# Kernel tuning notes

Measured on AMD Instinct MI355X. Metric: run time of the kernel, lower is better.

## Reference

```python
import jax, jax.numpy as jnp
import numpy as np

DIM = 512; NB = 4; BS = DIM // NB            # EinFFT blocks
DS = 64; DC = 4; EXP = 2; DI = EXP * DIM      # Mamba dims
DTR = DIM // 16                               # dt_rank
BLOCKS = 2; LAM = 0.01; B_SZ = 2; L_SZ = 1024

def layer_norm(x, w, b):
    m = x.mean(-1, keepdims=True)
    v = x.var(-1, keepdims=True)
    return (x - m) / jnp.sqrt(v + 1e-5) * w + b

def softshrink(x, lam):
    return jnp.where(x > lam, x - lam, jnp.where(x < -lam, x + lam, jnp.zeros((), x.dtype)))

def mamba(x, in_proj_w, conv_w, conv_b, x_proj_w, dt_proj_w, dt_proj_b, A_log, D, out_proj_w):
    B, L, _ = x.shape
    xz = x @ in_proj_w.T                      # (B,L,2*DI)
    xm, z = jnp.split(xz, 2, axis=-1)
    # causal depthwise conv1d, keep first L outputs
    xt = xm.transpose(0, 2, 1)                # (B,DI,L)
    conv = jax.lax.conv_general_dilated(xt, conv_w, (1,), [(DC - 1, 0)],
                                        feature_group_count=DI,
                                        dimension_numbers=('NCH', 'OIH', 'NCH'))
    xm = jax.nn.silu((conv + conv_b[None, :, None]).transpose(0, 2, 1))  # (B,L,DI)
    proj = xm @ x_proj_w.T                    # (B,L,DTR+2*DS)
    dt = proj[..., :DTR]
    Bm = proj[..., DTR:DTR + DS]
    Cm = proj[..., DTR + DS:]
    dt = jax.nn.softplus(dt @ dt_proj_w.T + dt_proj_b)   # (B,L,DI)
    A = -jnp.exp(A_log)                       # (DI,DS)

    def step(h, inp):
        dt_t, B_t, C_t, u_t = inp             # (B,DI),(B,DS),(B,DS),(B,DI)
        dA = jnp.exp(dt_t[:, :, None] * A)
        h = dA * h + dt_t[:, :, None] * B_t[:, None, :] * u_t[:, :, None]
        y = jnp.einsum('bds,bs->bd', h, C_t)
        return h, y

    h0 = jnp.zeros((B, DI, DS), x.dtype)
    _, ys = jax.lax.scan(step, h0, (dt.transpose(1, 0, 2), Bm.transpose(1, 0, 2),
                                    Cm.transpose(1, 0, 2), xm.transpose(1, 0, 2)))
    y = ys.transpose(1, 0, 2) + xm * D        # (B,L,DI)
    y = y * jax.nn.silu(z)
    return y @ out_proj_w.T

def einfft(x, cw1, cw2, cb1, cb2):
    B, N, C = x.shape
    xf = jnp.fft.fft2(x.reshape(B, N, NB, BS), axes=(1, 2), norm='ortho')
    mul = lambda t, w: jnp.einsum('BNbd,bdk->BNbk', t, w)
    r1 = jax.nn.relu(mul(xf.real, cw1[0]) - mul(xf.imag, cw1[1]) + cb1[0])
    i1 = jax.nn.relu(mul(xf.real, cw1[1]) + mul(xf.imag, cw1[0]) + cb1[1])
    r2 = softshrink(mul(r1, cw2[0]) - mul(i1, cw2[1]) + cb2[0], LAM)
    i2 = softshrink(mul(r1, cw2[1]) + mul(i1, cw2[0]) + cb2[1], LAM)
    out = jnp.fft.ifft2(r2 + 1j * i2, axes=(1, 2), norm='ortho')
    return out.real.astype(x.dtype).reshape(B, N, C)

def setup_inputs() -> dict:
    key = jax.random.key(0)
    ks = jax.random.split(key, 16)
    r = lambda i, shape, s: jax.random.normal(ks[i], shape, jnp.float32) * s
    A_log = jnp.log(jnp.tile(jnp.arange(1, DS + 1, dtype=jnp.float32), (DI, 1)))
    return {
        'x': jax.random.normal(ks[0], (B_SZ, L_SZ, DIM), jnp.float32),
        'ln_w': jnp.ones((DIM,), jnp.float32), 'ln_b': jnp.zeros((DIM,), jnp.float32),
        'in_proj_w': r(1, (2 * DI, DIM), 0.02),
        'conv_w': r(2, (DI, 1, DC), 0.1), 'conv_b': jnp.zeros((DI,), jnp.float32),
        'x_proj_w': r(3, (DTR + 2 * DS, DI), 0.02),
        'dt_proj_w': r(4, (DI, DTR), 0.02),
        'dt_proj_b': jnp.full((DI,), float(np.log(np.expm1(0.01))), jnp.float32),
        'A_log': A_log, 'D': jnp.ones((DI,), jnp.float32),
        'out_proj_w': r(5, (DIM, DI), 0.02),
        'norm2_w': jnp.ones((DIM,), jnp.float32), 'norm2_b': jnp.zeros((DIM,), jnp.float32),
        'cw1': r(6, (2, NB, BS, BS), 0.02), 'cw2': r(7, (2, NB, BS, BS), 0.02),
        'cb1': r(8, (2, NB, BS), 0.02), 'cb2': r(9, (2, NB, BS), 0.02),
    }

def reference(x, ln_w, ln_b, in_proj_w, conv_w, conv_b, x_proj_w, dt_proj_w, dt_proj_b,
              A_log, D, out_proj_w, norm2_w, norm2_b, cw1, cw2, cb1, cb2):
    for _ in range(BLOCKS):
        x = x + mamba(layer_norm(x, ln_w, ln_b), in_proj_w, conv_w, conv_b,
                      x_proj_w, dt_proj_w, dt_proj_b, A_log, D, out_proj_w)
        x = x + einfft(layer_norm(x, norm2_w, norm2_b), cw1, cw2, cb1, cb2)
    return x
```

## Files before the change

### kernel.cpp

```cpp
#include <hip/hip_runtime.h>

typedef unsigned short u16;
typedef __attribute__((ext_vector_type(8))) short bf8;
typedef __attribute__((ext_vector_type(4))) float f4;

__device__ __forceinline__ float bf2f(u16 b) {
    return __uint_as_float(((unsigned)b) << 16);
}
__device__ __forceinline__ u16 f2bf(float f) {
    unsigned u = __float_as_uint(f);
    u += 0x7fffu + ((u >> 16) & 1u);
    return (u16)(u >> 16);
}
__device__ __forceinline__ void pack8f(const float* v, u16* dst) {
    uint r0 = (uint)f2bf(v[0]) | ((uint)f2bf(v[1]) << 16);
    uint r1 = (uint)f2bf(v[2]) | ((uint)f2bf(v[3]) << 16);
    uint r2 = (uint)f2bf(v[4]) | ((uint)f2bf(v[5]) << 16);
    uint r3 = (uint)f2bf(v[6]) | ((uint)f2bf(v[7]) << 16);
    *(uint4*)dst = make_uint4(r0, r1, r2, r3);
}
__device__ __forceinline__ void pack8u(const u16* v, u16* dst) {
    uint r0 = (uint)v[0] | ((uint)v[1] << 16);
    uint r1 = (uint)v[2] | ((uint)v[3] << 16);
    uint r2 = (uint)v[4] | ((uint)v[5] << 16);
    uint r3 = (uint)v[6] | ((uint)v[7] << 16);
    *(uint4*)dst = make_uint4(r0, r1, r2, r3);
}
__device__ __forceinline__ bf8 neg8(bf8 v) {
    union { bf8 b; uint u[4]; } t; t.b = v;
    t.u[0] ^= 0x80008000u; t.u[1] ^= 0x80008000u;
    t.u[2] ^= 0x80008000u; t.u[3] ^= 0x80008000u;
    return t.b;
}

__global__ void detect_k(const u16* __restrict__ dtb, int* __restrict__ flag) {
    flag[0] = (dtb[0] == dtb[1] && dtb[1] == dtb[2] && dtb[2] == dtb[3] &&
               dtb[3] == dtb[4] && dtb[4] == dtb[5]) ? 1 : 0;
    flag[1] = 1;
}

__global__ __launch_bounds__(256)
void achk_k(const float* __restrict__ alog, int* __restrict__ flag) {
    int i = blockIdx.x * 256 + threadIdx.x;
    int s = i & 63;
    float n = __expf(alog[i]);
    float e = (float)(s + 1);
    if (fabsf(n - e) > 0.02f * e) atomicAnd(&flag[1], 0);
}

struct CvtArgs {
    const void* src[18];
    void* dst[18];
    int n[18];
    int obf[18];
};
__global__ __launch_bounds__(256)
void cvt_all_k(CvtArgs a, const int* __restrict__ flag) {
    const int t = blockIdx.y;
    const int n = a.n[t];
    const int f = flag[0];
    if (a.obf[t]) {
        u16* __restrict__ d = (u16*)a.dst[t];
        if (f) {
            const u16* __restrict__ s = (const u16*)a.src[t];
            for (int i = blockIdx.x * 256 + threadIdx.x; i < n; i += gridDim.x * 256)
                d[i] = s[i];
        } else {
            const float* __restrict__ s = (const float*)a.src[t];
            for (int i = blockIdx.x * 256 + threadIdx.x; i < n; i += gridDim.x * 256)
                d[i] = f2bf(s[i]);
        }
    } else {
        float* __restrict__ d = (float*)a.dst[t];
        if (f) {
            const u16* __restrict__ s = (const u16*)a.src[t];
            for (int i = blockIdx.x * 256 + threadIdx.x; i < n; i += gridDim.x * 256)
                d[i] = bf2f(s[i]);
        } else {
            const float* __restrict__ s = (const float*)a.src[t];
            for (int i = blockIdx.x * 256 + threadIdx.x; i < n; i += gridDim.x * 256)
                d[i] = s[i];
        }
    }
}

__global__ void out_k(const float* __restrict__ in, void* __restrict__ out,
                      int n, const int* __restrict__ flag) {
    int i = blockIdx.x * 256 + threadIdx.x;
    if (i >= n) return;
    if (flag[0]) ((u16*)out)[i] = f2bf(in[i]);
    else         ((float*)out)[i] = in[i];
}

__global__ void fgen_k(u16* __restrict__ Fr, u16* __restrict__ Fi) {
    int idx = blockIdx.x * 256 + threadIdx.x;
    int k = idx >> 10, n = idx & 1023;
    int m = (k * n) & 1023;
    float th = (float)m * (-6.283185307179586f / 1024.f);
    float s, c;
    __sincosf(th, &s, &c);
    Fr[idx] = f2bf(c * 0.03125f);
    Fi[idx] = f2bf(s * 0.03125f);
}

__global__ void wtr_k(const float* __restrict__ src, u16* __restrict__ dst) {
    int idx = blockIdx.x * 256 + threadIdx.x;
    int cin = idx & 127, cout = (idx >> 7) & 127, snb = idx >> 14;
    dst[(snb << 14) + (cout << 7) + cin] = f2bf(src[(snb << 14) + (cin << 7) + cout]);
}

__global__ __launch_bounds__(256)
void ln_k(const float* __restrict__ x, const float* __restrict__ w,
          const float* __restrict__ b, u16* __restrict__ out) {
    const int row = blockIdx.x, tid = threadIdx.x;
    const float* xr = x + (long)row * 512;
    float v0 = xr[tid], v1 = xr[tid + 256];
    float s = v0 + v1, q = v0 * v0 + v1 * v1;
#pragma unroll
    for (int off = 32; off; off >>= 1) {
        s += __shfl_xor(s, off);
        q += __shfl_xor(q, off);
    }
    __shared__ float ss[4], qq[4];
    int wid = tid >> 6;
    if ((tid & 63) == 0) { ss[wid] = s; qq[wid] = q; }
    __syncthreads();
    s = ss[0] + ss[1] + ss[2] + ss[3];
    q = qq[0] + qq[1] + qq[2] + qq[3];
    float mean = s * (1.f / 512.f);
    float var = q * (1.f / 512.f) - mean * mean;
    float rstd = rsqrtf(var + 1e-5f);
    u16* o = out + (long)row * 512;
    o[tid]       = f2bf((v0 - mean) * rstd * w[tid]       + b[tid]);
    o[tid + 256] = f2bf((v1 - mean) * rstd * w[tid + 256] + b[tid + 256]);
}

#define LSTR 40
template <int TAF, int EPI>
__global__ __launch_bounds__(256)
void mgemm_k(const void* __restrict__ Ap, const u16* __restrict__ Bp,
             float* __restrict__ D, int N, int K, int lda, int ldb, int ldc,
             const float* __restrict__ bias, const float* __restrict__ res) {
    const float* Af = (const float*)Ap;
    const u16*  Ab  = (const u16*)Ap;

    __shared__ u16 As[64 * LSTR];
    __shared__ u16 Bs[64 * LSTR];
    const int tid = threadIdx.x;
    const int lane = tid & 63;
    const int w = tid >> 6, wm = w & 1, wn = w >> 1;
    const int m0 = blockIdx.y * 64, n0 = blockIdx.x * 64;
    const int fr = (lane & 15), fq = (lane >> 4);

    f4 acc[2][2] = {};

    for (int k0 = 0; k0 < K; k0 += 32) {
        {
            const int ar = tid >> 2, aks = (tid & 3) << 3;
            if constexpr (TAF) {
                *(uint4*)&As[ar * LSTR + aks] =
                    *(const uint4*)(Ab + (long)(m0 + ar) * lda + k0 + aks);
            } else {
                const float* p = Af + (long)(m0 + ar) * lda + k0 + aks;
                float tv[8];
                float4 x = *(const float4*)p, y = *(const float4*)(p + 4);
                tv[0] = x.x; tv[1] = x.y; tv[2] = x.z; tv[3] = x.w;
                tv[4] = y.x; tv[5] = y.y; tv[6] = y.z; tv[7] = y.w;
                pack8f(tv, &As[ar * LSTR + aks]);
            }
        }
        {
            const int br = tid >> 2, bks = (tid & 3) << 3;
            uint4 raw = make_uint4(0, 0, 0, 0);
            if (n0 + br < N)
                raw = *(const uint4*)(Bp + (long)(n0 + br) * ldb + k0 + bks);
            *(uint4*)&Bs[br * LSTR + bks] = raw;
        }
        __syncthreads();
        bf8 af[2], bff[2];
#pragma unroll
        for (int t = 0; t < 2; t++) {
            af[t]  = *(bf8*)&As[(wm * 32 + t * 16 + fr) * LSTR + (fq << 3)];
            bff[t] = *(bf8*)&Bs[(wn * 32 + t * 16 + fr) * LSTR + (fq << 3)];
        }
#pragma unroll
        for (int i = 0; i < 2; i++)
#pragma unroll
            for (int j = 0; j < 2; j++)
                acc[i][j] = __builtin_amdgcn_mfma_f32_16x16x32_bf16(
                    af[i], bff[j], acc[i][j], 0, 0, 0);
        __syncthreads();
    }

#pragma unroll
    for (int i = 0; i < 2; i++) {
#pragma unroll
        for (int j = 0; j < 2; j++) {
            const int gmb = m0 + wm * 32 + i * 16 + (fq << 2);
            const int gn  = n0 + wn * 32 + j * 16 + fr;
            if (gn >= N) continue;
            float v[4];
#pragma unroll
            for (int e = 0; e < 4; e++) v[e] = acc[i][j][e];
            if constexpr (EPI == 1) {
                float bb = bias[gn];
#pragma unroll
                for (int e = 0; e < 4; e++) {
                    float t = v[e] + bb;
                    v[e] = (t > 20.f) ? t : log1pf(__expf(t));
                }
            }
#pragma unroll
            for (int e = 0; e < 4; e++) {
                long idx = (long)(gmb + e) * ldc + gn;
                float t = v[e];
                if constexpr (EPI == 2) t += res[idx];
                D[idx] = t;
            }
        }
    }
}

__global__ __launch_bounds__(256)
void dft_k(const u16* __restrict__ xn, const u16* __restrict__ Frb,
           const u16* __restrict__ Fib, float* __restrict__ XrA,
           float* __restrict__ XiA, float* __restrict__ XrB,
           float* __restrict__ XiB) {
    const int z = blockIdx.z, b = z >> 1, half = z & 1;
    const u16* A = xn + (long)b * 524288;
    float* Dr = (half ? XrB : XrA) + (long)b * 524288;
    float* Di = (half ? XiB : XiA) + (long)b * 524288;
    __shared__ u16 As[64 * LSTR], Brs[64 * LSTR], Bis[64 * LSTR];
    const int tid = threadIdx.x, lane = tid & 63;
    const int w = tid >> 6, wm = w & 1, wn = w >> 1;
    const int m0 = blockIdx.y * 64, n0 = blockIdx.x * 64;
    const int fr = (lane & 15), fq = (lane >> 4);
    const int kb = half * 512;
    f4 ar[2][2] = {}, ai[2][2] = {};

    for (int k0 = kb; k0 < kb + 512; k0 += 32) {
        {
            const int am = tid & 63, akb = (tid >> 6) << 3;
            u16 tv[8];
#pragma unroll
            for (int j = 0; j < 8; j++)
                tv[j] = A[(long)(k0 + akb + j) * 512 + m0 + am];
            pack8u(tv, &As[am * LSTR + akb]);
        }
        {
            const int br = tid >> 2, bks = (tid & 3) << 3;
            *(uint4*)&Brs[br * LSTR + bks] =
                *(const uint4*)(Frb + (long)(n0 + br) * 1024 + k0 + bks);
            *(uint4*)&Bis[br * LSTR + bks] =
                *(const uint4*)(Fib + (long)(n0 + br) * 1024 + k0 + bks);
        }
        __syncthreads();
        bf8 af[2], brf[2], bif[2];
#pragma unroll
        for (int t = 0; t < 2; t++) {
            af[t]  = *(bf8*)&As[(wm * 32 + t * 16 + fr) * LSTR + (fq << 3)];
            brf[t] = *(bf8*)&Brs[(wn * 32 + t * 16 + fr) * LSTR + (fq << 3)];
            bif[t] = *(bf8*)&Bis[(wn * 32 + t * 16 + fr) * LSTR + (fq << 3)];
        }
#pragma unroll
        for (int i = 0; i < 2; i++)
#pragma unroll
            for (int j = 0; j < 2; j++) {
                ar[i][j] = __builtin_amdgcn_mfma_f32_16x16x32_bf16(af[i], brf[j], ar[i][j], 0, 0, 0);
                ai[i][j] = __builtin_amdgcn_mfma_f32_16x16x32_bf16(af[i], bif[j], ai[i][j], 0, 0, 0);
            }
        __syncthreads();
    }
#pragma unroll
    for (int i = 0; i < 2; i++)
#pragma unroll
        for (int j = 0; j < 2; j++) {
            const int gmb = m0 + wm * 32 + i * 16 + (fq << 2);
            const int gn  = n0 + wn * 32 + j * 16 + fr;
#pragma unroll
            for (int e = 0; e < 4; e++) {
                Dr[(long)(gmb + e) * 1024 + gn] = ar[i][j][e];
                Di[(long)(gmb + e) * 1024 + gn] = ai[i][j][e];
            }
        }
}

__global__ __launch_bounds__(256)
void idft_k(const u16* __restrict__ Frb, const u16* __restrict__ Fib,
            const u16* __restrict__ X2r, const u16* __restrict__ X2i,
            float* __restrict__ P0, float* __restrict__ P1) {
    const int z = blockIdx.z, b = z >> 1, half = z & 1;
    const u16* Br = X2r + (long)b * 524288;
    const u16* Bi = X2i + (long)b * 524288;
    float* D = (half ? P1 : P0) + (long)b * 524288;
    __shared__ u16 Ars[64 * LSTR], Ais[64 * LSTR], Brs[64 * LSTR], Bis[64 * LSTR];
    const int tid = threadIdx.x, lane = tid & 63;
    const int w = tid >> 6, wm = w & 1, wn = w >> 1;
    const int m0 = blockIdx.y * 64, n0 = blockIdx.x * 64;
    const int fr = (lane & 15), fq = (lane >> 4);
    const int kb = half * 512;
    f4 acc[2][2] = {};

    for (int k0 = kb; k0 < kb + 512; k0 += 32) {
        const int ar = tid >> 2, aks = (tid & 3) << 3;
        *(uint4*)&Ars[ar * LSTR + aks] =
            *(const uint4*)(Frb + (long)(m0 + ar) * 1024 + k0 + aks);
        *(uint4*)&Ais[ar * LSTR + aks] =
            *(const uint4*)(Fib + (long)(m0 + ar) * 1024 + k0 + aks);
        *(uint4*)&Brs[ar * LSTR + aks] =
            *(const uint4*)(Br + (long)(n0 + ar) * 1024 + k0 + aks);
        *(uint4*)&Bis[ar * LSTR + aks] =
            *(const uint4*)(Bi + (long)(n0 + ar) * 1024 + k0 + aks);
        __syncthreads();
        bf8 fa[2], fb[2], xa[2], xb[2];
#pragma unroll
        for (int t = 0; t < 2; t++) {
            fa[t] = *(bf8*)&Ars[(wm * 32 + t * 16 + fr) * LSTR + (fq << 3)];
            fb[t] = *(bf8*)&Ais[(wm * 32 + t * 16 + fr) * LSTR + (fq << 3)];
            xa[t] = *(bf8*)&Brs[(wn * 32 + t * 16 + fr) * LSTR + (fq << 3)];
            xb[t] = *(bf8*)&Bis[(wn * 32 + t * 16 + fr) * LSTR + (fq << 3)];
        }
#pragma unroll
        for (int i = 0; i < 2; i++)
#pragma unroll
            for (int j = 0; j < 2; j++) {
                acc[i][j] = __builtin_amdgcn_mfma_f32_16x16x32_bf16(fa[i], xa[j], acc[i][j], 0, 0, 0);
                acc[i][j] = __builtin_amdgcn_mfma_f32_16x16x32_bf16(fb[i], xb[j], acc[i][j], 0, 0, 0);
            }
        __syncthreads();
    }
#pragma unroll
    for (int i = 0; i < 2; i++)
#pragma unroll
        for (int j = 0; j < 2; j++) {
            const int gmb = m0 + wm * 32 + i * 16 + (fq << 2);
            const int gn  = n0 + wn * 32 + j * 16 + fr;
#pragma unroll
            for (int e = 0; e < 4; e++)
                D[(long)(gmb + e) * 512 + gn] = acc[i][j][e];
        }
}

__global__ __launch_bounds__(256)
void addres_k(float* __restrict__ xbuf, const float* __restrict__ P0,
              const float* __restrict__ P1) {
    int i = (blockIdx.x * 256 + threadIdx.x) << 2;
    float4 a = *(const float4*)(xbuf + i);
    float4 p = *(const float4*)(P0 + i);
    float4 q = *(const float4*)(P1 + i);
    *(float4*)(xbuf + i) = make_float4(a.x + p.x + q.x, a.y + p.y + q.y,
                                       a.z + p.z + q.z, a.w + p.w + q.w);
}

template <int ACT>
__global__ __launch_bounds__(256)
void cmix_k(const u16* __restrict__ Xr, const u16* __restrict__ Xi,
            const u16* __restrict__ WT, const float* __restrict__ cb,
            u16* __restrict__ Or, u16* __restrict__ Oi) {
    const int z = blockIdx.z, b = z >> 2, nb = z & 3;
    const u16* Ar = Xr + (long)b * 524288 + nb * 131072;
    const u16* Ai = Xi + (long)b * 524288 + nb * 131072;
    const u16* Wr = WT + nb * 16384;
    const u16* Wi = WT + 65536 + nb * 16384;
    u16* Dr = Or + (long)b * 524288 + nb * 131072;
    u16* Di = Oi + (long)b * 524288 + nb * 131072;
    __shared__ u16 Ars[64 * LSTR], Ais[64 * LSTR], Brs[64 * LSTR], Bis[64 * LSTR];
    const int tid = threadIdx.x, lane = tid & 63;
    const int w = tid >> 6, wm = w & 1, wn = w >> 1;
    const int m0 = blockIdx.y * 64, n0 = blockIdx.x * 64;
    const int fr = (lane & 15), fq = (lane >> 4);
    f4 accr[2][2] = {}, acci[2][2] = {};

    for (int k0 = 0; k0 < 128; k0 += 32) {
        {
            const int am = tid & 63, akb = (tid >> 6) << 3;
            u16 tr[8], ti[8];
#pragma unroll
            for (int j = 0; j < 8; j++) {
                long off = (long)(k0 + akb + j) * 1024 + m0 + am;
                tr[j] = Ar[off]; ti[j] = Ai[off];
            }
            pack8u(tr, &Ars[am * LSTR + akb]);
            pack8u(ti, &Ais[am * LSTR + akb]);
        }
        {
            const int br = tid >> 2, bks = (tid & 3) << 3;
            *(uint4*)&Brs[br * LSTR + bks] =
                *(const uint4*)(Wr + (long)(n0 + br) * 128 + k0 + bks);
            *(uint4*)&Bis[br * LSTR + bks] =
                *(const uint4*)(Wi + (long)(n0 + br) * 128 + k0 + bks);
        }
        __syncthreads();
        bf8 arf[2], aif[2], brf[2], bif[2];
#pragma unroll
        for (int t = 0; t < 2; t++) {
            arf[t] = *(bf8*)&Ars[(wm * 32 + t * 16 + fr) * LSTR + (fq << 3)];
            aif[t] = *(bf8*)&Ais[(wm * 32 + t * 16 + fr) * LSTR + (fq << 3)];
            brf[t] = *(bf8*)&Brs[(wn * 32 + t * 16 + fr) * LSTR + (fq << 3)];
            bif[t] = *(bf8*)&Bis[(wn * 32 + t * 16 + fr) * LSTR + (fq << 3)];
        }
        bf8 nai[2] = { neg8(aif[0]), neg8(aif[1]) };
#pragma unroll
        for (int i = 0; i < 2; i++)
#pragma unroll
            for (int j = 0; j < 2; j++) {
                accr[i][j] = __builtin_amdgcn_mfma_f32_16x16x32_bf16(arf[i], brf[j], accr[i][j], 0, 0, 0);
                accr[i][j] = __builtin_amdgcn_mfma_f32_16x16x32_bf16(nai[i], bif[j], accr[i][j], 0, 0, 0);
                acci[i][j] = __builtin_amdgcn_mfma_f32_16x16x32_bf16(arf[i], bif[j], acci[i][j], 0, 0, 0);
                acci[i][j] = __builtin_amdgcn_mfma_f32_16x16x32_bf16(aif[i], brf[j], acci[i][j], 0, 0, 0);
            }
        __syncthreads();
    }
#pragma unroll
    for (int i = 0; i < 2; i++)
#pragma unroll
        for (int j = 0; j < 2; j++) {
            const int gmb = m0 + wm * 32 + i * 16 + (fq << 2);
            const int gn  = n0 + wn * 32 + j * 16 + fr;
            const float bbr = cb[nb * 128 + gn];
            const float bbi = cb[512 + nb * 128 + gn];
            u16 pr[4], pi[4];
#pragma unroll
            for (int e = 0; e < 4; e++) {
                float vr = accr[i][j][e] + bbr;
                float vi = acci[i][j][e] + bbi;
                if (ACT == 0) {
                    vr = fmaxf(vr, 0.f);
                    vi = fmaxf(vi, 0.f);
                } else {
                    vr = (vr > 0.01f) ? vr - 0.01f : ((vr < -0.01f) ? vr + 0.01f : 0.f);
                    vi = (vi > 0.01f) ? vi - 0.01f : ((vi < -0.01f) ? vi + 0.01f : 0.f);
                }
                pr[e] = f2bf(vr); pi[e] = f2bf(vi);
            }
            uint2 wr2, wi2;
            wr2.x = (uint)pr[0] | ((uint)pr[1] << 16);
            wr2.y = (uint)pr[2] | ((uint)pr[3] << 16);
            wi2.x = (uint)pi[0] | ((uint)pi[1] << 16);
            wi2.y = (uint)pi[2] | ((uint)pi[3] << 16);
            *(uint2*)&Dr[(long)gn * 1024 + gmb] = wr2;
            *(uint2*)&Di[(long)gn * 1024 + gmb] = wi2;
        }
}

__global__ __launch_bounds__(256)
void conv_k(const float* __restrict__ xz, const float* __restrict__ cw,
            const float* __restrict__ cb, float* __restrict__ u) {
    int idx = blockIdx.x * 256 + threadIdx.x;
    int d = idx & 1023;
    int l = (idx >> 10) & 1023;
    int b = idx >> 20;
    float acc = cb[d];
    const float* base = xz + (long)b * 1024 * 2048 + d;
#pragma unroll
    for (int j = 0; j < 4; j++) {
        int li = l - 3 + j;
        if (li >= 0) acc = fmaf(cw[d * 4 + j], base[(long)li * 2048], acc);
    }
    float sig = 1.f / (1.f + __expf(-acc));
    u[idx] = acc * sig;
}


__global__ __launch_bounds__(256)
void scan1_k(const float* __restrict__ dtL, const float* __restrict__ uL,
             const float* __restrict__ projL, const float* __restrict__ alog,
             u16* __restrict__ Hb, float* __restrict__ Sbuf,
             const int* __restrict__ flag) {
    const int dg = blockIdx.x, c = blockIdx.y, b = blockIdx.z;
    const int tid = threadIdx.x;
    const int d = dg * 256 + tid;
    const int t0 = c * 16;
    __shared__ float Bls[16][64];
    {
        int r = tid >> 4, cg = (tid & 15) << 2;
        *(float4*)&Bls[r][cg] =
            *(const float4*)(projL + ((long)(b * 1024 + t0 + r)) * 160 + 32 + cg);
    }
    __syncthreads();

    float h[64];
#pragma unroll
    for (int s = 0; s < 64; s++) h[s] = 0.f;
    float S = 0.f;
    const float* dtp = dtL + (long)(b * 1024 + t0) * 1024 + d;
    const float* up  = uL  + (long)(b * 1024 + t0) * 1024 + d;

    if (flag[1]) {
        for (int t = 0; t < 16; ++t) {
            float dt = dtp[(long)t * 1024];
            float uu = up[(long)t * 1024];
            float dtu = dt * uu;
            S += dt;
            float q = __expf(-dt);
            float q2 = q * q, q3 = q2 * q, q4 = q2 * q2;
            float a0 = q, a1 = q2, a2 = q3, a3 = q4;
            const float4* B4p = (const float4*)&Bls[t][0];
#pragma unroll
            for (int sg = 0; sg < 16; ++sg) {
                float4 B4 = B4p[sg];
                h[sg * 4 + 0] = a0 * h[sg * 4 + 0] + dtu * B4.x;
                h[sg * 4 + 1] = a1 * h[sg * 4 + 1] + dtu * B4.y;
                h[sg * 4 + 2] = a2 * h[sg * 4 + 2] + dtu * B4.z;
                h[sg * 4 + 3] = a3 * h[sg * 4 + 3] + dtu * B4.w;
                a0 *= q4; a1 *= q4; a2 *= q4; a3 *= q4;
            }
        }
    } else {
        float A[64];
        const float* ap = alog + (long)d * 64;
#pragma unroll
        for (int s = 0; s < 64; s += 4) {
            float4 a4 = *(const float4*)(ap + s);
            A[s] = -__expf(a4.x); A[s + 1] = -__expf(a4.y);
            A[s + 2] = -__expf(a4.z); A[s + 3] = -__expf(a4.w);
        }
        for (int t = 0; t < 16; ++t) {
            float dt = dtp[(long)t * 1024];
            float uu = up[(long)t * 1024];
            float dtu = dt * uu;
            S += dt;
            const float4* B4p = (const float4*)&Bls[t][0];
#pragma unroll
            for (int sg = 0; sg < 16; ++sg) {
                float4 B4 = B4p[sg];
                h[sg * 4 + 0] = __expf(dt * A[sg * 4 + 0]) * h[sg * 4 + 0] + dtu * B4.x;
                h[sg * 4 + 1] = __expf(dt * A[sg * 4 + 1]) * h[sg * 4 + 1] + dtu * B4.y;
                h[sg * 4 + 2] = __expf(dt * A[sg * 4 + 2]) * h[sg * 4 + 2] + dtu * B4.z;
                h[sg * 4 + 3] = __expf(dt * A[sg * 4 + 3]) * h[sg * 4 + 3] + dtu * B4.w;
            }
        }
    }
    u16* Hp = Hb + ((((long)(b * 64 + c)) * 1024 + d) << 6);
#pragma unroll
    for (int s = 0; s < 64; s += 4) {
        uint2 p;
        p.x = ((__float_as_uint(h[s]) + 0x8000u) >> 16) |
              ((__float_as_uint(h[s + 1]) + 0x8000u) & 0xFFFF0000u);
        p.y = ((__float_as_uint(h[s + 2]) + 0x8000u) >> 16) |
              ((__float_as_uint(h[s + 3]) + 0x8000u) & 0xFFFF0000u);
        *(uint2*)&Hp[s] = p;
    }
    Sbuf[(b * 64 + c) * 1024 + d] = S;
}

__global__ __launch_bounds__(256)
void scan2_k(const float* __restrict__ alog, const float* __restrict__ Sbuf,
             u16* __restrict__ Hb) {
    int idx = blockIdx.x * 256 + threadIdx.x;
    int s = idx & 63, d = (idx >> 6) & 1023, b = idx >> 16;
    float A = -__expf(alog[(long)d * 64 + s]);
    float carry = 0.f;
    for (int c = 0; c < 64; ++c) {
        float S = Sbuf[(b * 64 + c) * 1024 + d];
        float P = __expf(A * S);
        long off = ((((long)(b * 64 + c)) * 1024 + d) << 6) + s;
        float H = bf2f(Hb[off]);
        Hb[off] = (u16)((__float_as_uint(carry) + 0x8000u) >> 16);
        carry = P * carry + H;
    }
}

__global__ __launch_bounds__(256)
void scan3_k(float* __restrict__ dtL, const float* __restrict__ uL,
             const float* __restrict__ xz, const float* __restrict__ projL,
             const float* __restrict__ alog, const u16* __restrict__ Hb,
             const float* __restrict__ Dw, const int* __restrict__ flag) {
    const int dg = blockIdx.x, c = blockIdx.y, b = blockIdx.z;
    const int tid = threadIdx.x;
    const int d = dg * 256 + tid;
    const int t0 = c * 16;
    __shared__ float Bls[16][64];
    __shared__ float Cls[16][64];
    {
        int r = tid >> 4, cg = (tid & 15) << 2;
        const float* src = projL + ((long)(b * 1024 + t0 + r)) * 160 + 32 + cg;
        *(float4*)&Bls[r][cg] = *(const float4*)src;
        *(float4*)&Cls[r][cg] = *(const float4*)(src + 64);
    }
    __syncthreads();

    float h[64];
    const u16* Hp = Hb + ((((long)(b * 64 + c)) * 1024 + d) << 6);
#pragma unroll
    for (int s = 0; s < 64; s += 4) {
        uint2 p = *(const uint2*)&Hp[s];
        h[s]     = __uint_as_float(p.x << 16);
        h[s + 1] = __uint_as_float(p.x & 0xFFFF0000u);
        h[s + 2] = __uint_as_float(p.y << 16);
        h[s + 3] = __uint_as_float(p.y & 0xFFFF0000u);
    }
    const float Dd = Dw[d];
    float* dtp = dtL + (long)(b * 1024 + t0) * 1024 + d;
    const float* up = uL + (long)(b * 1024 + t0) * 1024 + d;
    const float* zp = xz + (long)(b * 1024 + t0) * 2048 + 1024 + d;

    if (flag[1]) {
        for (int t = 0; t < 16; ++t) {
            float dt = dtp[(long)t * 1024];
            float uu = up[(long)t * 1024];
            float zz = zp[(long)t * 2048];
            float dtu = dt * uu;
            float y = 0.f;
            float q = __expf(-dt);
            float q2 = q * q, q3 = q2 * q, q4 = q2 * q2;
            float a0 = q, a1 = q2, a2 = q3, a3 = q4;
            const float4* B4p = (const float4*)&Bls[t][0];
            const float4* C4p = (const float4*)&Cls[t][0];
#pragma unroll
            for (int sg = 0; sg < 16; ++sg) {
                float4 B4 = B4p[sg];
                float4 C4 = C4p[sg];
                h[sg * 4 + 0] = a0 * h[sg * 4 + 0] + dtu * B4.x;
                y = fmaf(h[sg * 4 + 0], C4.x, y);
                h[sg * 4 + 1] = a1 * h[sg * 4 + 1] + dtu * B4.y;
                y = fmaf(h[sg * 4 + 1], C4.y, y);
                h[sg * 4 + 2] = a2 * h[sg * 4 + 2] + dtu * B4.z;
                y = fmaf(h[sg * 4 + 2], C4.z, y);
                h[sg * 4 + 3] = a3 * h[sg * 4 + 3] + dtu * B4.w;
                y = fmaf(h[sg * 4 + 3], C4.w, y);
                a0 *= q4; a1 *= q4; a2 *= q4; a3 *= q4;
            }
            float g = zz / (1.f + __expf(-zz));
            dtp[(long)t * 1024] = (y + uu * Dd) * g;
        }
    } else {
        float A[64];
        const float* ap = alog + (long)d * 64;
#pragma unroll
        for (int s = 0; s < 64; s += 4) {
            float4 a4 = *(const float4*)(ap + s);
            A[s] = -__expf(a4.x); A[s + 1] = -__expf(a4.y);
            A[s + 2] = -__expf(a4.z); A[s + 3] = -__expf(a4.w);
        }
        for (int t = 0; t < 16; ++t) {
            float dt = dtp[(long)t * 1024];
            float uu = up[(long)t * 1024];
            float zz = zp[(long)t * 2048];
            float dtu = dt * uu;
            float y = 0.f;
            const float4* B4p = (const float4*)&Bls[t][0];
            const float4* C4p = (const float4*)&Cls[t][0];
#pragma unroll
            for (int sg = 0; sg < 16; ++sg) {
                float4 B4 = B4p[sg];
                float4 C4 = C4p[sg];
                h[sg * 4 + 0] = __expf(dt * A[sg * 4 + 0]) * h[sg * 4 + 0] + dtu * B4.x;
                y = fmaf(h[sg * 4 + 0], C4.x, y);
                h[sg * 4 + 1] = __expf(dt * A[sg * 4 + 1]) * h[sg * 4 + 1] + dtu * B4.y;
                y = fmaf(h[sg * 4 + 1], C4.y, y);
                h[sg * 4 + 2] = __expf(dt * A[sg * 4 + 2]) * h[sg * 4 + 2] + dtu * B4.z;
                y = fmaf(h[sg * 4 + 2], C4.z, y);
                h[sg * 4 + 3] = __expf(dt * A[sg * 4 + 3]) * h[sg * 4 + 3] + dtu * B4.w;
                y = fmaf(h[sg * 4 + 3], C4.w, y);
            }
            float g = zz / (1.f + __expf(-zz));
            dtp[(long)t * 1024] = (y + uu * Dd) * g;
        }
    }
}

__global__ __launch_bounds__(256)
void fft4_k(const float* __restrict__ XrA, const float* __restrict__ XiA,
            const float* __restrict__ XrB, const float* __restrict__ XiB,
            u16* __restrict__ Orb, u16* __restrict__ Oib) {
    int idx = blockIdx.x * 256 + threadIdx.x;
    int kf = idx & 1023, c = (idx >> 10) & 127, b = idx >> 17;
    long base = (long)b * 524288 + (long)c * 1024 + kf;
    const int S = 131072;
    float r0 = XrA[base] + XrB[base];
    float r1 = XrA[base + S] + XrB[base + S];
    float r2 = XrA[base + 2 * S] + XrB[base + 2 * S];
    float r3 = XrA[base + 3 * S] + XrB[base + 3 * S];
    float i0 = XiA[base] + XiB[base];
    float i1 = XiA[base + S] + XiB[base + S];
    float i2 = XiA[base + 2 * S] + XiB[base + 2 * S];
    float i3 = XiA[base + 3 * S] + XiB[base + 3 * S];
    Orb[base]         = f2bf((r0 + r1 + r2 + r3) * 0.5f);
    Oib[base]         = f2bf((i0 + i1 + i2 + i3) * 0.5f);
    Orb[base + S]     = f2bf((r0 + i1 - r2 - i3) * 0.5f);
    Oib[base + S]     = f2bf((i0 - r1 - i2 + r3) * 0.5f);
    Orb[base + 2 * S] = f2bf((r0 - r1 + r2 - r3) * 0.5f);
    Oib[base + 2 * S] = f2bf((i0 - i1 + i2 - i3) * 0.5f);
    Orb[base + 3 * S] = f2bf((r0 - i1 - r2 + i3) * 0.5f);
    Oib[base + 3 * S] = f2bf((i0 + r1 - i2 - r3) * 0.5f);
}

__global__ __launch_bounds__(256)
void ifft4_k(u16* __restrict__ Xr, u16* __restrict__ Xi) {
    int idx = blockIdx.x * 256 + threadIdx.x;
    int kf = idx & 1023, c = (idx >> 10) & 127, b = idx >> 17;
    long base = (long)b * 524288 + (long)c * 1024 + kf;
    const int S = 131072;
    float r0 = bf2f(Xr[base]), r1 = bf2f(Xr[base + S]),
          r2 = bf2f(Xr[base + 2 * S]), r3 = bf2f(Xr[base + 3 * S]);
    float i0 = bf2f(Xi[base]), i1 = bf2f(Xi[base + S]),
          i2 = bf2f(Xi[base + 2 * S]), i3 = bf2f(Xi[base + 3 * S]);
    Xr[base]         = f2bf((r0 + r1 + r2 + r3) * 0.5f);
    Xi[base]         = f2bf((i0 + i1 + i2 + i3) * 0.5f);
    Xr[base + S]     = f2bf((r0 - i1 - r2 + i3) * 0.5f);
    Xi[base + S]     = f2bf((i0 + r1 - i2 - r3) * 0.5f);
    Xr[base + 2 * S] = f2bf((r0 - r1 + r2 - r3) * 0.5f);
    Xi[base + 2 * S] = f2bf((i0 - i1 + i2 - i3) * 0.5f);
    Xr[base + 3 * S] = f2bf((r0 + i1 - r2 - i3) * 0.5f);
    Xi[base + 3 * S] = f2bf((i0 - r1 - i2 + r3) * 0.5f);
}

extern "C" void kernel_launch(void* const* d_in, const int* in_sizes, int n_in,
                              void* d_out, int out_size, void* d_ws, size_t ws_size,
                              hipStream_t stream) {
    float* ws = (float*)d_ws;
    int* flag = (int*)ws;
    size_t o = 64;
    float* xbuf  = ws + o; o += 1048576;
    float* xz    = ws + o; o += 4194304;
    float* dtL   = ws + o; o += 2097152;
    float* uL    = ws + o; o += 2097152;
    float* projL = ws + o; o += 327680;
    u16* xnb     = (u16*)(ws + o); o += 524288;
    u16* Frb     = (u16*)(ws + o); o += 524288;
    u16* Fib     = (u16*)(ws + o); o += 524288;
    u16* wInpB   = (u16*)(ws + o); o += 524288;
    u16* wXpB    = (u16*)(ws + o); o += 81920;
    u16* wDtB    = (u16*)(ws + o); o += 16384;
    u16* wOutB   = (u16*)(ws + o); o += 262144;
    u16* WT1     = (u16*)(ws + o); o += 65536;
    u16* WT2     = (u16*)(ws + o); o += 65536;
    float* wCw1f = ws + o; o += 131072;
    float* wCw2f = ws + o; o += 131072;
    float* wConv = ws + o; o += 4096;
    float* wAlog = ws + o; o += 65536;
    float* wLnW  = ws + o; o += 512;
    float* wLnB  = ws + o; o += 512;
    float* wConvB= ws + o; o += 1024;
    float* wDtBias=ws + o; o += 1024;
    float* wD    = ws + o; o += 1024;
    float* wN2w  = ws + o; o += 512;
    float* wN2b  = ws + o; o += 512;
    float* wCb1  = ws + o; o += 1024;
    float* wCb2  = ws + o; o += 1024;
    float* Hreg  = ws + o; o += 4194304;
    float* Sbuf  = ws + o; o += 131072;
    u16* Hb    = (u16*)Hreg;
    float* XrA = dtL;
    float* XiA = uL;
    float* XrB = Hreg;
    float* XiB = Hreg + 1048576;
    float* P0  = dtL;
    float* P1  = uL;
    u16* xzb  = (u16*)xz;
    u16* Xrb  = xzb;
    u16* Xib  = xzb + 1048576;
    u16* r1b  = xzb + 2097152;
    u16* i1b  = xzb + 3145728;
    u16* X2rb = xzb + 4194304;
    u16* X2ib = xzb + 5242880;

    dim3 blk(256);

    detect_k<<<1, 1, 0, stream>>>((const u16*)d_in[8], flag);

    CvtArgs ca;
    void* dsts[18] = {xbuf, wLnW, wLnB, wInpB, wConv, wConvB, wXpB, wDtB, wDtBias,
                      wAlog, wD, wOutB, wN2w, wN2b, wCw1f, wCw2f, wCb1, wCb2};
    int obf[18]    = {0,    0,    0,    1,     0,     0,      1,    1,    0,
                      0,     0,  1,     0,    0,    0,     0,     0,    0};
    for (int i = 0; i < 18; i++) {
        ca.src[i] = d_in[i];
        ca.dst[i] = dsts[i];
        ca.n[i] = in_sizes[i];
        ca.obf[i] = obf[i];
    }
    cvt_all_k<<<dim3(64, 18), blk, 0, stream>>>(ca, flag);
    achk_k<<<256, blk, 0, stream>>>(wAlog, flag);
    fgen_k<<<4096, blk, 0, stream>>>(Frb, Fib);
    wtr_k<<<512, blk, 0, stream>>>(wCw1f, WT1);
    wtr_k<<<512, blk, 0, stream>>>(wCw2f, WT2);

    for (int it = 0; it < 2; ++it) {
        ln_k<<<2048, blk, 0, stream>>>(xbuf, wLnW, wLnB, xnb);
        mgemm_k<1, 0><<<dim3(32, 32), blk, 0, stream>>>(
            xnb, wInpB, xz, 2048, 512, 512, 512, 2048, nullptr, nullptr);
        conv_k<<<8192, blk, 0, stream>>>(xz, wConv, wConvB, uL);
        mgemm_k<0, 0><<<dim3(3, 32), blk, 0, stream>>>(
            uL, wXpB, projL, 160, 1024, 1024, 1024, 160, nullptr, nullptr);
        mgemm_k<0, 1><<<dim3(16, 32), blk, 0, stream>>>(
            projL, wDtB, dtL, 1024, 32, 160, 32, 1024, wDtBias, nullptr);
        scan1_k<<<dim3(4, 64, 2), blk, 0, stream>>>(dtL, uL, projL, wAlog, Hb, Sbuf, flag);
        scan2_k<<<512, blk, 0, stream>>>(wAlog, Sbuf, Hb);
        scan3_k<<<dim3(4, 64, 2), blk, 0, stream>>>(dtL, uL, xz, projL, wAlog, Hb, wD, flag);
        mgemm_k<0, 2><<<dim3(8, 32), blk, 0, stream>>>(
            dtL, wOutB, xbuf, 512, 1024, 1024, 1024, 512, nullptr, xbuf);

        ln_k<<<2048, blk, 0, stream>>>(xbuf, wN2w, wN2b, xnb);
        dft_k<<<dim3(16, 8, 4), blk, 0, stream>>>(xnb, Frb, Fib, XrA, XiA, XrB, XiB);
        fft4_k<<<1024, blk, 0, stream>>>(XrA, XiA, XrB, XiB, Xrb, Xib);
        cmix_k<0><<<dim3(2, 16, 8), blk, 0, stream>>>(Xrb, Xib, WT1, wCb1, r1b, i1b);
        cmix_k<1><<<dim3(2, 16, 8), blk, 0, stream>>>(r1b, i1b, WT2, wCb2, X2rb, X2ib);
        ifft4_k<<<1024, blk, 0, stream>>>(X2rb, X2ib);
        idft_k<<<dim3(8, 16, 4), blk, 0, stream>>>(Frb, Fib, X2rb, X2ib, P0, P1);
        addres_k<<<1024, blk, 0, stream>>>(xbuf, P0, P1);
    }

    out_k<<<(out_size + 255) / 256, blk, 0, stream>>>(xbuf, d_out, out_size, flag);
}
```

Before: 528.4 us.

## Replace dense DFT matmuls over sequence axis with in-LDS radix-2 FFT

The length-1024 DFT along the sequence axis was a bf16 MFMA GEMM against precomputed twiddle matrices, split into two K halves. It is replaced by one workgroup per (batch, channel) running a 10-stage radix-2 FFT in shared memory with padded indexing. The inverse is handled the same way, followed by a tiled transpose-add into the residual. This drops the O(N^2) work and the twiddle-matrix generation, at the cost of ten barrier-separated LDS stages, strided global loads, and an extra transpose pass.

```diff
diff --git a/kernel.cpp b/kernel.cpp
--- a/kernel.cpp
+++ b/kernel.cpp
@@ -92,17 +92,6 @@
     else         ((float*)out)[i] = in[i];
 }
 
-__global__ void fgen_k(u16* __restrict__ Fr, u16* __restrict__ Fi) {
-    int idx = blockIdx.x * 256 + threadIdx.x;
-    int k = idx >> 10, n = idx & 1023;
-    int m = (k * n) & 1023;
-    float th = (float)m * (-6.283185307179586f / 1024.f);
-    float s, c;
-    __sincosf(th, &s, &c);
-    Fr[idx] = f2bf(c * 0.03125f);
-    Fi[idx] = f2bf(s * 0.03125f);
-}
-
 __global__ void wtr_k(const float* __restrict__ src, u16* __restrict__ dst) {
     int idx = blockIdx.x * 256 + threadIdx.x;
     int cin = idx & 127, cout = (idx >> 7) & 127, snb = idx >> 14;
@@ -222,134 +211,147 @@
 }
 
 __global__ __launch_bounds__(256)
-void dft_k(const u16* __restrict__ xn, const u16* __restrict__ Frb,
-           const u16* __restrict__ Fib, float* __restrict__ XrA,
-           float* __restrict__ XiA, float* __restrict__ XrB,
-           float* __restrict__ XiB) {
-    const int z = blockIdx.z, b = z >> 1, half = z & 1;
-    const u16* A = xn + (long)b * 524288;
-    float* Dr = (half ? XrB : XrA) + (long)b * 524288;
-    float* Di = (half ? XiB : XiA) + (long)b * 524288;
-    __shared__ u16 As[64 * LSTR], Brs[64 * LSTR], Bis[64 * LSTR];
-    const int tid = threadIdx.x, lane = tid & 63;
-    const int w = tid >> 6, wm = w & 1, wn = w >> 1;
-    const int m0 = blockIdx.y * 64, n0 = blockIdx.x * 64;
-    const int fr = (lane & 15), fq = (lane >> 4);
-    const int kb = half * 512;
-    f4 ar[2][2] = {}, ai[2][2] = {};
-
-    for (int k0 = kb; k0 < kb + 512; k0 += 32) {
-        {
-            const int am = tid & 63, akb = (tid >> 6) << 3;
-            u16 tv[8];
-#pragma unroll
-            for (int j = 0; j < 8; j++)
-                tv[j] = A[(long)(k0 + akb + j) * 512 + m0 + am];
-            pack8u(tv, &As[am * LSTR + akb]);
-        }
-        {
-            const int br = tid >> 2, bks = (tid & 3) << 3;
-            *(uint4*)&Brs[br * LSTR + bks] =
-                *(const uint4*)(Frb + (long)(n0 + br) * 1024 + k0 + bks);
-            *(uint4*)&Bis[br * LSTR + bks] =
-                *(const uint4*)(Fib + (long)(n0 + br) * 1024 + k0 + bks);
-        }
+void fftn_k(const u16* __restrict__ xn, float* __restrict__ Xr,
+            float* __restrict__ Xi) {
+    const int bc = blockIdx.x;
+    const int b = bc >> 9, c = bc & 511;
+    const int tid = threadIdx.x;
+    __shared__ float re[1056], im[1056], twr[512], twi[512];
+#pragma unroll
+    for (int r = 0; r < 2; ++r) {
+        int k = tid + r * 256;
+        float s, cc;
+        __sincosf((float)k * -6.1359231515425649e-3f, &s, &cc);
+        twr[k] = cc; twi[k] = s;
+    }
+    const u16* src = xn + ((long)b * 1024) * 512 + c;
+#pragma unroll
+    for (int r = 0; r < 4; ++r) {
+        int n = tid + r * 256;
+        float v = bf2f(src[(long)n * 512]);
+        int a = n + (n >> 5);
+        re[a] = v; im[a] = 0.f;
+    }
+#pragma unroll
+    for (int lh = 9; lh >= 0; --lh) {
         __syncthreads();
-        bf8 af[2], brf[2], bif[2];
-#pragma unroll
-        for (int t = 0; t < 2; t++) {
-            af[t]  = *(bf8*)&As[(wm * 32 + t * 16 + fr) * LSTR + (fq << 3)];
-            brf[t] = *(bf8*)&Brs[(wn * 32 + t * 16 + fr) * LSTR + (fq << 3)];
-            bif[t] = *(bf8*)&Bis[(wn * 32 + t * 16 + fr) * LSTR + (fq << 3)];
-        }
-#pragma unroll
-        for (int i = 0; i < 2; i++)
-#pragma unroll
-            for (int j = 0; j < 2; j++) {
-                ar[i][j] = __builtin_amdgcn_mfma_f32_16x16x32_bf16(af[i], brf[j], ar[i][j], 0, 0, 0);
-                ai[i][j] = __builtin_amdgcn_mfma_f32_16x16x32_bf16(af[i], bif[j], ai[i][j], 0, 0, 0);
-            }
+        const int half = 1 << lh;
+#pragma unroll
+        for (int r = 0; r < 2; ++r) {
+            int j = tid + r * 256;
+            int p = j & (half - 1);
+            int i0 = ((j >> lh) << (lh + 1)) | p;
+            int i1 = i0 + half;
+            int a0 = i0 + (i0 >> 5), a1 = i1 + (i1 >> 5);
+            float ar = re[a0], ai = im[a0];
+            float br = re[a1], bi = im[a1];
+            int tn = p << (9 - lh);
+            float wr = twr[tn], wi = twi[tn];
+            re[a0] = ar + br; im[a0] = ai + bi;
+            float tr = ar - br, ti = ai - bi;
+            re[a1] = tr * wr - ti * wi;
+            im[a1] = tr * wi + ti * wr;
+        }
+    }
+    __syncthreads();
+    float* dr = Xr + (long)bc * 1024;
+    float* di = Xi + (long)bc * 1024;
+#pragma unroll
+    for (int r = 0; r < 4; ++r) {
+        int kf = tid + r * 256;
+        int sidx = __brev((unsigned)kf) >> 22;
+        int a = sidx + (sidx >> 5);
+        dr[kf] = re[a] * 0.03125f;
+        di[kf] = im[a] * 0.03125f;
+    }
+}
+
+__global__ __launch_bounds__(256)
+void ifftn_k(const u16* __restrict__ X2r, const u16* __restrict__ X2i,
+             float* __restrict__ Yc) {
+    const int bc = blockIdx.x;
+    const int tid = threadIdx.x;
+    __shared__ float re[1056], im[1056], twr[512], twi[512];
+#pragma unroll
+    for (int r = 0; r < 2; ++r) {
+        int k = tid + r * 256;
+        float s, cc;
+        __sincosf((float)k * 6.1359231515425649e-3f, &s, &cc);
+        twr[k] = cc; twi[k] = s;
+    }
+    const u16* sr = X2r + (long)bc * 1024;
+    const u16* si = X2i + (long)bc * 1024;
+    {
+        int k4 = tid * 4;
+        uint2 pr = *(const uint2*)&sr[k4];
+        uint2 pi = *(const uint2*)&si[k4];
+        u16 rv[4] = {(u16)(pr.x & 0xFFFF), (u16)(pr.x >> 16),
+                     (u16)(pr.y & 0xFFFF), (u16)(pr.y >> 16)};
+        u16 iv[4] = {(u16)(pi.x & 0xFFFF), (u16)(pi.x >> 16),
+                     (u16)(pi.y & 0xFFFF), (u16)(pi.y >> 16)};
+#pragma unroll
+        for (int e = 0; e < 4; ++e) {
+            int idx = k4 + e;
+            int a = idx + (idx >> 5);
+            re[a] = bf2f(rv[e]);
+            im[a] = bf2f(iv[e]);
+        }
+    }
+#pragma unroll
+    for (int lh = 9; lh >= 0; --lh) {
         __syncthreads();
-    }
-#pragma unroll
-    for (int i = 0; i < 2; i++)
-#pragma unroll
-        for (int j = 0; j < 2; j++) {
-            const int gmb = m0 + wm * 32 + i * 16 + (fq << 2);
-            const int gn  = n0 + wn * 32 + j * 16 + fr;
-#pragma unroll
-            for (int e = 0; e < 4; e++) {
-                Dr[(long)(gmb + e) * 1024 + gn] = ar[i][j][e];
-                Di[(long)(gmb + e) * 1024 + gn] = ai[i][j][e];
-            }
-        }
-}
-
-__global__ __launch_bounds__(256)
-void idft_k(const u16* __restrict__ Frb, const u16* __restrict__ Fib,
-            const u16* __restrict__ X2r, const u16* __restrict__ X2i,
-            float* __restrict__ P0, float* __restrict__ P1) {
-    const int z = blockIdx.z, b = z >> 1, half = z & 1;
-    const u16* Br = X2r + (long)b * 524288;
-    const u16* Bi = X2i + (long)b * 524288;
-    float* D = (half ? P1 : P0) + (long)b * 524288;
-    __shared__ u16 Ars[64 * LSTR], Ais[64 * LSTR], Brs[64 * LSTR], Bis[64 * LSTR];
-    const int tid = threadIdx.x, lane = tid & 63;
-    const int w = tid >> 6, wm = w & 1, wn = w >> 1;
-    const int m0 = blockIdx.y * 64, n0 = blockIdx.x * 64;
-    const int fr = (lane & 15), fq = (lane >> 4);
-    const int kb = half * 512;
-    f4 acc[2][2] = {};
-
-    for (int k0 = kb; k0 < kb + 512; k0 += 32) {
-        const int ar = tid >> 2, aks = (tid & 3) << 3;
-        *(uint4*)&Ars[ar * LSTR + aks] =
-            *(const uint4*)(Frb + (long)(m0 + ar) * 1024 + k0 + aks);
-        *(uint4*)&Ais[ar * LSTR + aks] =
-            *(const uint4*)(Fib + (long)(m0 + ar) * 1024 + k0 + aks);
-        *(uint4*)&Brs[ar * LSTR + aks] =
-            *(const uint4*)(Br + (long)(n0 + ar) * 1024 + k0 + aks);
-        *(uint4*)&Bis[ar * LSTR + aks] =
-            *(const uint4*)(Bi + (long)(n0 + ar) * 1024 + k0 + aks);
-        __syncthreads();
-        bf8 fa[2], fb[2], xa[2], xb[2];
-#pragma unroll
-        for (int t = 0; t < 2; t++) {
-            fa[t] = *(bf8*)&Ars[(wm * 32 + t * 16 + fr) * LSTR + (fq << 3)];
-            fb[t] = *(bf8*)&Ais[(wm * 32 + t * 16 + fr) * LSTR + (fq << 3)];
-            xa[t] = *(bf8*)&Brs[(wn * 32 + t * 16 + fr) * LSTR + (fq << 3)];
-            xb[t] = *(bf8*)&Bis[(wn * 32 + t * 16 + fr) * LSTR + (fq << 3)];
-        }
-#pragma unroll
-        for (int i = 0; i < 2; i++)
-#pragma unroll
-            for (int j = 0; j < 2; j++) {
-                acc[i][j] = __builtin_amdgcn_mfma_f32_16x16x32_bf16(fa[i], xa[j], acc[i][j], 0, 0, 0);
-                acc[i][j] = __builtin_amdgcn_mfma_f32_16x16x32_bf16(fb[i], xb[j], acc[i][j], 0, 0, 0);
-            }
-        __syncthreads();
-    }
-#pragma unroll
-    for (int i = 0; i < 2; i++)
-#pragma unroll
-        for (int j = 0; j < 2; j++) {
-            const int gmb = m0 + wm * 32 + i * 16 + (fq << 2);
-            const int gn  = n0 + wn * 32 + j * 16 + fr;
-#pragma unroll
-            for (int e = 0; e < 4; e++)
-                D[(long)(gmb + e) * 512 + gn] = acc[i][j][e];
-        }
-}
-
-__global__ __launch_bounds__(256)
-void addres_k(float* __restrict__ xbuf, const float* __restrict__ P0,
-              const float* __restrict__ P1) {
-    int i = (blockIdx.x * 256 + threadIdx.x) << 2;
-    float4 a = *(const float4*)(xbuf + i);
-    float4 p = *(const float4*)(P0 + i);
-    float4 q = *(const float4*)(P1 + i);
-    *(float4*)(xbuf + i) = make_float4(a.x + p.x + q.x, a.y + p.y + q.y,
-                                       a.z + p.z + q.z, a.w + p.w + q.w);
+        const int half = 1 << lh;
+#pragma unroll
+        for (int r = 0; r < 2; ++r) {
+            int j = tid + r * 256;
+            int p = j & (half - 1);
+            int i0 = ((j >> lh) << (lh + 1)) | p;
+            int i1 = i0 + half;
+            int a0 = i0 + (i0 >> 5), a1 = i1 + (i1 >> 5);
+            float ar = re[a0], ai = im[a0];
+            float br = re[a1], bi = im[a1];
+            int tn = p << (9 - lh);
+            float wr = twr[tn], wi = twi[tn];
+            re[a0] = ar + br; im[a0] = ai + bi;
+            float tr = ar - br, ti = ai - bi;
+            re[a1] = tr * wr - ti * wi;
+            im[a1] = tr * wi + ti * wr;
+        }
+    }
+    __syncthreads();
+    float* d = Yc + (long)bc * 1024;
+#pragma unroll
+    for (int r = 0; r < 4; ++r) {
+        int n = tid + r * 256;
+        int sidx = __brev((unsigned)n) >> 22;
+        int a = sidx + (sidx >> 5);
+        d[n] = re[a] * 0.03125f;
+    }
+}
+
+__global__ __launch_bounds__(256)
+void transadd_k(float* __restrict__ xbuf, const float* __restrict__ Yc) {
+    const int b = blockIdx.z;
+    const int c0 = blockIdx.x * 64, n0 = blockIdx.y * 64;
+    __shared__ float T[64][65];
+    const int tid = threadIdx.x;
+    const int r = tid >> 2, q = (tid & 3) * 16;
+    const float* src = Yc + ((long)(b * 512 + c0 + r)) * 1024 + n0 + q;
+#pragma unroll
+    for (int k = 0; k < 4; ++k) {
+        float4 v = *(const float4*)(src + k * 4);
+        T[r][q + k * 4 + 0] = v.x; T[r][q + k * 4 + 1] = v.y;
+        T[r][q + k * 4 + 2] = v.z; T[r][q + k * 4 + 3] = v.w;
+    }
+    __syncthreads();
+    float* dst = xbuf + ((long)(b * 1024 + n0 + r)) * 512 + c0 + q;
+#pragma unroll
+    for (int k = 0; k < 4; ++k) {
+        float4 w = *(const float4*)(dst + k * 4);
+        w.x += T[q + k * 4 + 0][r]; w.y += T[q + k * 4 + 1][r];
+        w.z += T[q + k * 4 + 2][r]; w.w += T[q + k * 4 + 3][r];
+        *(float4*)(dst + k * 4) = w;
+    }
 }
 
 template <int ACT>
@@ -461,7 +463,6 @@
     u[idx] = acc * sig;
 }
 
-
 __global__ __launch_bounds__(256)
 void scan1_k(const float* __restrict__ dtL, const float* __restrict__ uL,
              const float* __restrict__ projL, const float* __restrict__ alog,
@@ -661,21 +662,14 @@
 }
 
 __global__ __launch_bounds__(256)
-void fft4_k(const float* __restrict__ XrA, const float* __restrict__ XiA,
-            const float* __restrict__ XrB, const float* __restrict__ XiB,
+void fft4_k(const float* __restrict__ Xr, const float* __restrict__ Xi,
             u16* __restrict__ Orb, u16* __restrict__ Oib) {
     int idx = blockIdx.x * 256 + threadIdx.x;
     int kf = idx & 1023, c = (idx >> 10) & 127, b = idx >> 17;
     long base = (long)b * 524288 + (long)c * 1024 + kf;
     const int S = 131072;
-    float r0 = XrA[base] + XrB[base];
-    float r1 = XrA[base + S] + XrB[base + S];
-    float r2 = XrA[base + 2 * S] + XrB[base + 2 * S];
-    float r3 = XrA[base + 3 * S] + XrB[base + 3 * S];
-    float i0 = XiA[base] + XiB[base];
-    float i1 = XiA[base + S] + XiB[base + S];
-    float i2 = XiA[base + 2 * S] + XiB[base + 2 * S];
-    float i3 = XiA[base + 3 * S] + XiB[base + 3 * S];
+    float r0 = Xr[base], r1 = Xr[base + S], r2 = Xr[base + 2 * S], r3 = Xr[base + 3 * S];
+    float i0 = Xi[base], i1 = Xi[base + S], i2 = Xi[base + 2 * S], i3 = Xi[base + 3 * S];
     Orb[base]         = f2bf((r0 + r1 + r2 + r3) * 0.5f);
     Oib[base]         = f2bf((i0 + i1 + i2 + i3) * 0.5f);
     Orb[base + S]     = f2bf((r0 + i1 - r2 - i3) * 0.5f);
@@ -718,8 +712,6 @@
     float* uL    = ws + o; o += 2097152;
     float* projL = ws + o; o += 327680;
     u16* xnb     = (u16*)(ws + o); o += 524288;
-    u16* Frb     = (u16*)(ws + o); o += 524288;
-    u16* Fib     = (u16*)(ws + o); o += 524288;
     u16* wInpB   = (u16*)(ws + o); o += 524288;
     u16* wXpB    = (u16*)(ws + o); o += 81920;
     u16* wDtB    = (u16*)(ws + o); o += 16384;
@@ -742,12 +734,9 @@
     float* Hreg  = ws + o; o += 4194304;
     float* Sbuf  = ws + o; o += 131072;
     u16* Hb    = (u16*)Hreg;
-    float* XrA = dtL;
-    float* XiA = uL;
-    float* XrB = Hreg;
-    float* XiB = Hreg + 1048576;
-    float* P0  = dtL;
-    float* P1  = uL;
+    float* Xr  = dtL;
+    float* Xi  = uL;
+    float* Yc  = dtL;
     u16* xzb  = (u16*)xz;
     u16* Xrb  = xzb;
     u16* Xib  = xzb + 1048576;
@@ -773,7 +762,6 @@
     }
     cvt_all_k<<<dim3(64, 18), blk, 0, stream>>>(ca, flag);
     achk_k<<<256, blk, 0, stream>>>(wAlog, flag);
-    fgen_k<<<4096, blk, 0, stream>>>(Frb, Fib);
     wtr_k<<<512, blk, 0, stream>>>(wCw1f, WT1);
     wtr_k<<<512, blk, 0, stream>>>(wCw2f, WT2);
 
@@ -793,13 +781,13 @@
             dtL, wOutB, xbuf, 512, 1024, 1024, 1024, 512, nullptr, xbuf);
 
         ln_k<<<2048, blk, 0, stream>>>(xbuf, wN2w, wN2b, xnb);
-        dft_k<<<dim3(16, 8, 4), blk, 0, stream>>>(xnb, Frb, Fib, XrA, XiA, XrB, XiB);
-        fft4_k<<<1024, blk, 0, stream>>>(XrA, XiA, XrB, XiB, Xrb, Xib);
+        fftn_k<<<1024, blk, 0, stream>>>(xnb, Xr, Xi);
+        fft4_k<<<1024, blk, 0, stream>>>(Xr, Xi, Xrb, Xib);
         cmix_k<0><<<dim3(2, 16, 8), blk, 0, stream>>>(Xrb, Xib, WT1, wCb1, r1b, i1b);
         cmix_k<1><<<dim3(2, 16, 8), blk, 0, stream>>>(r1b, i1b, WT2, wCb2, X2rb, X2ib);
         ifft4_k<<<1024, blk, 0, stream>>>(X2rb, X2ib);
-        idft_k<<<dim3(8, 16, 4), blk, 0, stream>>>(Frb, Fib, X2rb, X2ib, P0, P1);
-        addres_k<<<1024, blk, 0, stream>>>(xbuf, P0, P1);
+        ifftn_k<<<1024, blk, 0, stream>>>(X2rb, X2ib, Yc);
+        transadd_k<<<dim3(8, 16, 2), blk, 0, stream>>>(xbuf, Yc);
     }
 
     out_k<<<(out_size + 255) / 256, blk, 0, stream>>>(xbuf, d_out, out_size, flag);
```

After: 507.3 us. 1.04x faster.
